# Kernel optimization log

Measured on AMD Instinct MI355X. Metric: run time of the kernel, lower is better.

The kernel has to match this reference:

```python
import jax, jax.numpy as jnp
import numpy as np

IN_DIM = 64
OUT_DIM = 128
GROUPS = 4
KS = 3
PAD = 1
SPLINE_ORDER = 3
GRID_SIZE = 5
GRID_K = GRID_SIZE + SPLINE_ORDER  # 8
GRID_LO, GRID_HI = -1.0, 1.0
_H = (GRID_HI - GRID_LO) / GRID_SIZE
GRID = jnp.linspace(GRID_LO - _H * SPLINE_ORDER, GRID_HI + _H * SPLINE_ORDER,
                    GRID_SIZE + 2 * SPLINE_ORDER + 1, dtype=jnp.float32)  # [14]
EPS = 1e-5


def _conv(x, w):
    # NCHW x OIHW -> NCHW, stride 1, dilation 1, padding PAD
    return jax.lax.conv_general_dilated(
        x, w, window_strides=(1, 1), padding=((PAD, PAD), (PAD, PAD)),
        dimension_numbers=('NCHW', 'OIHW', 'NCHW'))


def _bspline_bases(x):
    # Cox-de-Boor recursion; x: [B,C,H,W] -> [B, C*GRID_K, H, W]
    xu = x[..., None]  # [B,C,H,W,1]
    g = GRID
    bases = ((xu >= g[:-1]) & (xu < g[1:])).astype(x.dtype)  # [B,C,H,W,13]
    for k in range(1, SPLINE_ORDER + 1):
        left = g[:-(k + 1)]
        right = g[k:-1]
        delta = jnp.where(right == left, jnp.ones_like(right), right - left)
        bases = ((xu - left) / delta * bases[..., :-1]
                 + (g[k + 1:] - xu) / (g[k + 1:] - g[1:-k]) * bases[..., 1:])
    B, C, H, W, K = bases.shape  # K == GRID_K
    # moveaxis(-1, 2) then flatten(1, 2): channel-major, basis-minor ordering
    return jnp.moveaxis(bases, -1, 2).reshape(B, C * K, H, W)


def setup_inputs() -> dict:
    key = jax.random.key(0)
    k1, k2 = jax.random.split(key)
    x = jax.random.normal(k1, (8, IN_DIM, 64, 64), dtype=jnp.float32)
    # layer_weight: [out/g, (in/g)*(grid_k+1), ks, ks] = [32, 144, 3, 3]
    layer_weight = jax.random.normal(
        k2, (OUT_DIM // GROUPS, (IN_DIM // GROUPS) * (GRID_K + 1), KS, KS),
        dtype=jnp.float32) * 0.05
    prelu_w = jnp.full((GROUPS,), 0.25, dtype=jnp.float32)  # torch PReLU init
    return {"x": x, "layer_weight": layer_weight, "prelu_w": prelu_w}


def reference(x, layer_weight, prelu_w):
    cin_g = IN_DIM // GROUPS
    cout_g = OUT_DIM // GROUPS
    base_w = layer_weight[:, -cin_g:].reshape(cout_g, cin_g, KS, KS)
    spline_w = layer_weight[:, :-cin_g].reshape(cout_g, cin_g * GRID_K, KS, KS)
    outs = []
    for g in range(GROUPS):
        xg = x[:, g * cin_g:(g + 1) * cin_g]
        base_out = _conv(jax.nn.gelu(xg, approximate=False), base_w)
        spline_out = _conv(_bspline_bases(xg), spline_w)
        y = base_out + spline_out
        # InstanceNorm2d (affine=False): per-sample per-channel spatial norm
        mu = y.mean(axis=(2, 3), keepdims=True)
        var = y.var(axis=(2, 3), keepdims=True)
        y = (y - mu) / jnp.sqrt(var + EPS)
        # PReLU with scalar slope per group
        y = jnp.where(y >= 0, y, prelu_w[g] * y)
        outs.append(y)
    return jnp.concatenate(outs, axis=1)  # [B, OUT_DIM, H, W]
```

## Files before the change

kernel.cpp:

```cpp
#include <hip/hip_runtime.h>
#include <hip/hip_bf16.h>
#include <math.h>

typedef __attribute__((ext_vector_type(8))) short short8;
typedef __attribute__((ext_vector_type(4))) float f32x4;
typedef __attribute__((ext_vector_type(16))) float f32x16;
typedef unsigned int u32;
typedef unsigned long long u64;

__device__ __forceinline__ ushort f2bf(float f) {
    u32 u = __float_as_uint(f);
    return (ushort)((u + 0x7fffu + ((u >> 16) & 1u)) >> 16);
}

__global__ void wtrans(const float* __restrict__ lw, ushort* __restrict__ w2) {
    int t = blockIdx.x * 256 + threadIdx.x;
    if (t >= 5184) return;
    int l    = t & 63;
    int page = t >> 6;
    int ks  = page % 9;
    int tap = page / 9;
    int oc = l & 31;
    int kbase = ks * 16 + ((l >> 5) << 3);
    short8 v;
#pragma unroll
    for (int e = 0; e < 8; ++e) {
        int k = kbase + e;
        v[e] = (short)f2bf(lw[(oc * 144 + k) * 9 + tap]);
    }
    ((short8*)w2)[t] = v;
}

__global__ __launch_bounds__(256, 4) void kanconv(const float* __restrict__ x,
                                                  const ushort* __restrict__ w2,
                                                  ushort* __restrict__ yraw) {
    __shared__ __align__(16) ushort Fs[108 * 152];
    const int tid  = threadIdx.x;
    const int tile = blockIdx.x;
    const int b    = blockIdx.y;
    const int g    = blockIdx.z;
    const int h0 = (tile >> 2) * 4;
    const int w0 = (tile & 3) * 16;
    const float* xg = x + ((size_t)(b * 64 + g * 16)) * 4096;

    float xv[7];
    unsigned imgbits = 0;
#pragma unroll
    for (int it = 0; it < 7; ++it) {
        int e = it * 256 + tid;
        float v = 0.f;
        if (e < 1728) {
            int icg = e / 108;
            int p   = e - icg * 108;
            int py = p / 18, px = p - py * 18;
            int hy = h0 + py - 1, wx = w0 + px - 1;
            if (((unsigned)hy < 64u) && ((unsigned)wx < 64u)) {
                v = xg[icg * 4096 + hy * 64 + wx];
                imgbits |= (1u << it);
            }
        }
        xv[it] = v;
    }

#pragma unroll
    for (int it = 0; it < 7; ++it) {
        int e = it * 256 + tid;
        if (e < 1728) {
            int icg = e / 108;
            int p   = e - icg * 108;
            bool img = (imgbits >> it) & 1u;
            float v = xv[it];
            float tpos = (v + 2.2f) * 2.5f;
            float cf = floorf(tpos);
            int ci = (int)cf;
            float u = tpos - cf;
            float u2 = u * u, u3 = u2 * u, om = 1.f - u;
            const float s6 = 1.f / 6.f;
            float q0 = om * om * om * s6;
            float q1 = (4.f - 6.f * u2 + 3.f * u3) * s6;
            float q2 = (1.f + 3.f * u + 3.f * u2 - 3.f * u3) * s6;
            float q3 = u3 * s6;
            u64 Q =   (u64)f2bf(q0)
                    | ((u64)f2bf(q1) << 16)
                    | ((u64)f2bf(q2) << 32)
                    | ((u64)f2bf(q3) << 48);
            u64 lo = 0, hi = 0;
            if (img && ci >= 0 && ci <= 10) {
                int s = ci * 16 - 48;
                if (s < 0)        { lo = Q >> (-s); }
                else if (s < 64)  { lo = Q << s; hi = s ? (Q >> (64 - s)) : 0ull; }
                else              { hi = Q << (s - 64); }
            }
            union { u64 u64v[2]; short8 s8; } un;
            un.u64v[0] = lo; un.u64v[1] = hi;
            ushort* row = &Fs[p * 152];
            *(short8*)(row + icg * 8) = un.s8;
            float z  = v * 0.70710678118654752f;
            float az = fabsf(z);
            float tt = 1.f / fmaf(0.3275911f, az, 1.f);
            float poly = tt * fmaf(tt, fmaf(tt, fmaf(tt, fmaf(tt, 1.061405429f,
                          -1.453152027f), 1.421413741f), -0.284496736f),
                          0.254829592f);
            float er = 1.f - poly * __expf(-z * z);
            er = (z < 0.f) ? -er : er;
            float ge = 0.5f * v * (1.f + er);
            row[128 + icg] = f2bf(ge);
        }
    }
    __syncthreads();

    const int wv = tid >> 6;
    const int l  = tid & 63;
    const int la = l & 31, klo = l >> 5;
    const int p0row = la >> 4, p0col = la & 15;

    f32x16 accA, accB;
#pragma unroll
    for (int i = 0; i < 16; ++i) { accA[i] = 0.f; accB[i] = 0.f; }
    const short8* w8 = (const short8*)w2;

#pragma unroll
    for (int t2 = 0; t2 < 2; ++t2) {
        const int tap = wv * 2 + t2;
        const int kh = tap / 3, kw = tap - kh * 3;
        const ushort* fb0 = &Fs[((p0row + kh) * 18 + (p0col + kw)) * 152 + klo * 8];
        const ushort* fb1 = fb0 + 2 * 18 * 152;
        const short8* ap = w8 + tap * 576 + l;
#pragma unroll
        for (int ks = 0; ks < 9; ++ks) {
            short8 a   = ap[ks * 64];
            short8 bf0 = *(const short8*)(fb0 + ks * 16);
            short8 bf1 = *(const short8*)(fb1 + ks * 16);
            accA = __builtin_amdgcn_mfma_f32_32x32x16_bf16(a, bf0, accA, 0, 0, 0);
            accB = __builtin_amdgcn_mfma_f32_32x32x16_bf16(a, bf1, accB, 0, 0, 0);
        }
    }
    if (wv == 3) {
        const ushort* fb0 = &Fs[((p0row + 2) * 18 + (p0col + 2)) * 152 + klo * 8];
        const ushort* fb1 = fb0 + 2 * 18 * 152;
        const short8* ap = w8 + 8 * 576 + l;
#pragma unroll
        for (int ks = 0; ks < 9; ++ks) {
            short8 a   = ap[ks * 64];
            short8 bf0 = *(const short8*)(fb0 + ks * 16);
            short8 bf1 = *(const short8*)(fb1 + ks * 16);
            accA = __builtin_amdgcn_mfma_f32_32x32x16_bf16(a, bf0, accA, 0, 0, 0);
            accB = __builtin_amdgcn_mfma_f32_32x32x16_bf16(a, bf1, accB, 0, 0, 0);
        }
    }

    __syncthreads();
    float* comb = (float*)Fs;
    if (wv != 0) {
        float* cp = comb + ((wv - 1) * 64 + l) * 20;
        *(f32x4*)(cp + 0)  = f32x4{accA[0], accA[1], accA[2], accA[3]};
        *(f32x4*)(cp + 4)  = f32x4{accA[4], accA[5], accA[6], accA[7]};
        *(f32x4*)(cp + 8)  = f32x4{accA[8], accA[9], accA[10], accA[11]};
        *(f32x4*)(cp + 12) = f32x4{accA[12], accA[13], accA[14], accA[15]};
    }
    if (wv != 1) {
        int slot = (wv == 0) ? 3 : (2 + wv);
        float* cp = comb + (slot * 64 + l) * 20;
        *(f32x4*)(cp + 0)  = f32x4{accB[0], accB[1], accB[2], accB[3]};
        *(f32x4*)(cp + 4)  = f32x4{accB[4], accB[5], accB[6], accB[7]};
        *(f32x4*)(cp + 8)  = f32x4{accB[8], accB[9], accB[10], accB[11]};
        *(f32x4*)(cp + 12) = f32x4{accB[12], accB[13], accB[14], accB[15]};
    }
    __syncthreads();
    if (wv < 2) {
        f32x16 sum = (wv == 0) ? accA : accB;
        const int sbase = (wv == 0) ? 0 : 3;
#pragma unroll
        for (int s = 0; s < 3; ++s) {
            const float* cp = comb + ((sbase + s) * 64 + l) * 20;
            f32x4 c0 = *(const f32x4*)(cp + 0);
            f32x4 c1 = *(const f32x4*)(cp + 4);
            f32x4 c2 = *(const f32x4*)(cp + 8);
            f32x4 c3 = *(const f32x4*)(cp + 12);
#pragma unroll
            for (int r = 0; r < 4; ++r) {
                sum[r]      += c0[r];
                sum[r + 4]  += c1[r];
                sum[r + 8]  += c2[r];
                sum[r + 12] += c3[r];
            }
        }
        const int pix = wv * 32 + la;
        const int prow = pix >> 4, pcol = pix & 15;
        ushort* yb = yraw + (((size_t)b * 128 + g * 32) * 64 + h0 + prow) * 64
                          + w0 + pcol;
#pragma unroll
        for (int r = 0; r < 16; ++r) {
            int oc = (r & 3) + 8 * (r >> 2) + 4 * klo;
            yb[(size_t)oc * 4096] = f2bf(sum[r]);
        }
    }
}

__global__ __launch_bounds__(256) void instnorm(const ushort* __restrict__ yraw,
                                                float* __restrict__ y,
                                                const float* __restrict__ prelu) {
    const int blk = blockIdx.x;
    const int tid = threadIdx.x;
    const short8* rp = (const short8*)(yraw + (size_t)blk * 4096);
    short8 a = rp[tid * 2], c = rp[tid * 2 + 1];
    float v[16];
#pragma unroll
    for (int j = 0; j < 8; ++j) {
        v[j]     = __uint_as_float(((u32)(ushort)a[j]) << 16);
        v[8 + j] = __uint_as_float(((u32)(ushort)c[j]) << 16);
    }
    float s = 0.f, s2 = 0.f;
#pragma unroll
    for (int j = 0; j < 16; ++j) { s += v[j]; s2 += v[j] * v[j]; }
#pragma unroll
    for (int off = 32; off > 0; off >>= 1) {
        s  += __shfl_down(s, off);
        s2 += __shfl_down(s2, off);
    }
    __shared__ float red[8];
    int wave = tid >> 6;
    if ((tid & 63) == 0) { red[wave] = s; red[4 + wave] = s2; }
    __syncthreads();
    float S  = red[0] + red[1] + red[2] + red[3];
    float S2 = red[4] + red[5] + red[6] + red[7];
    float mean = S * (1.0f / 4096.0f);
    float var  = S2 * (1.0f / 4096.0f) - mean * mean;
    float rstd = rsqrtf(var + 1e-5f);
    float slope = prelu[(blk >> 5) & 3];
    float4* op = (float4*)(y + (size_t)blk * 4096) + tid * 4;
#pragma unroll
    for (int k = 0; k < 4; ++k) {
        float4 o;
        float t;
        t = (v[k * 4 + 0] - mean) * rstd; o.x = t >= 0.f ? t : slope * t;
        t = (v[k * 4 + 1] - mean) * rstd; o.y = t >= 0.f ? t : slope * t;
        t = (v[k * 4 + 2] - mean) * rstd; o.z = t >= 0.f ? t : slope * t;
        t = (v[k * 4 + 3] - mean) * rstd; o.w = t >= 0.f ? t : slope * t;
        op[k] = o;
    }
}

extern "C" void kernel_launch(void* const* d_in, const int* in_sizes, int n_in,
                              void* d_out, int out_size, void* d_ws, size_t ws_size,
                              hipStream_t stream) {
    const float* x     = (const float*)d_in[0];
    const float* lw    = (const float*)d_in[1];
    const float* prelu = (const float*)d_in[2];
    float*  out  = (float*)d_out;
    ushort* w2   = (ushort*)d_ws;
    ushort* yraw = (ushort*)((char*)d_ws + 92160);

    wtrans<<<21, 256, 0, stream>>>(lw, w2);
    dim3 grid(64, 8, 4);
    kanconv<<<grid, 256, 0, stream>>>(x, w2, yraw);
    instnorm<<<1024, 256, 0, stream>>>(yraw, out, prelu);
}
```

Before: 40.70 us.

## Split input channels across blocks and sum bf16 partials in instnorm

```diff
diff --git a/kernel.cpp b/kernel.cpp
--- a/kernel.cpp
+++ b/kernel.cpp
@@ -12,44 +12,53 @@
     u32 u = __float_as_uint(f);
     return (ushort)((u + 0x7fffu + ((u >> 16) & 1u)) >> 16);
 }
+__device__ __forceinline__ float bf2f(ushort h) {
+    return __uint_as_float(((u32)h) << 16);
+}
 
 __global__ void wtrans(const float* __restrict__ lw, ushort* __restrict__ w2) {
     int t = blockIdx.x * 256 + threadIdx.x;
-    if (t >= 5184) return;
+    if (t >= 5760) return;
     int l    = t & 63;
     int page = t >> 6;
-    int ks  = page % 9;
-    int tap = page / 9;
+    int ks  = page % 5;
+    int tap = (page / 5) % 9;
+    int kk  = page / 45;
     int oc = l & 31;
     int kbase = ks * 16 + ((l >> 5) << 3);
     short8 v;
 #pragma unroll
     for (int e = 0; e < 8; ++e) {
         int k = kbase + e;
-        v[e] = (short)f2bf(lw[(oc * 144 + k) * 9 + tap]);
+        float val = 0.f;
+        if (k < 64)       val = lw[(oc * 144 + kk * 64 + k) * 9 + tap];
+        else if (k < 72)  val = lw[(oc * 144 + 128 + kk * 8 + (k - 64)) * 9 + tap];
+        v[e] = (short)f2bf(val);
     }
     ((short8*)w2)[t] = v;
 }
 
-__global__ __launch_bounds__(256, 4) void kanconv(const float* __restrict__ x,
+__global__ __launch_bounds__(128, 4) void kanconv(const float* __restrict__ x,
                                                   const ushort* __restrict__ w2,
                                                   ushort* __restrict__ yraw) {
-    __shared__ __align__(16) ushort Fs[108 * 152];
+    __shared__ __align__(16) ushort Fs[108 * 88];
     const int tid  = threadIdx.x;
     const int tile = blockIdx.x;
     const int b    = blockIdx.y;
-    const int g    = blockIdx.z;
+    const int gz   = blockIdx.z;
+    const int g    = gz & 3;
+    const int kk   = gz >> 2;
     const int h0 = (tile >> 2) * 4;
     const int w0 = (tile & 3) * 16;
-    const float* xg = x + ((size_t)(b * 64 + g * 16)) * 4096;
+    const float* xg = x + ((size_t)(b * 64 + g * 16 + kk * 8)) * 4096;
 
     float xv[7];
     unsigned imgbits = 0;
 #pragma unroll
     for (int it = 0; it < 7; ++it) {
-        int e = it * 256 + tid;
+        int e = it * 128 + tid;
         float v = 0.f;
-        if (e < 1728) {
+        if (e < 864) {
             int icg = e / 108;
             int p   = e - icg * 108;
             int py = p / 18, px = p - py * 18;
@@ -64,8 +73,8 @@
 
 #pragma unroll
     for (int it = 0; it < 7; ++it) {
-        int e = it * 256 + tid;
-        if (e < 1728) {
+        int e = it * 128 + tid;
+        if (e < 864) {
             int icg = e / 108;
             int p   = e - icg * 108;
             bool img = (imgbits >> it) & 1u;
@@ -93,7 +102,7 @@
             }
             union { u64 u64v[2]; short8 s8; } un;
             un.u64v[0] = lo; un.u64v[1] = hi;
-            ushort* row = &Fs[p * 152];
+            ushort* row = &Fs[p * 88];
             *(short8*)(row + icg * 8) = un.s8;
             float z  = v * 0.70710678118654752f;
             float az = fabsf(z);
@@ -104,96 +113,45 @@
             float er = 1.f - poly * __expf(-z * z);
             er = (z < 0.f) ? -er : er;
             float ge = 0.5f * v * (1.f + er);
-            row[128 + icg] = f2bf(ge);
+            row[64 + icg] = f2bf(ge);
         }
+    }
+    {
+        short8 z8 = {0, 0, 0, 0, 0, 0, 0, 0};
+        if (tid < 108) *(short8*)&Fs[tid * 88 + 72] = z8;
     }
     __syncthreads();
 
     const int wv = tid >> 6;
     const int l  = tid & 63;
     const int la = l & 31, klo = l >> 5;
-    const int p0row = la >> 4, p0col = la & 15;
-
-    f32x16 accA, accB;
-#pragma unroll
-    for (int i = 0; i < 16; ++i) { accA[i] = 0.f; accB[i] = 0.f; }
-    const short8* w8 = (const short8*)w2;
-
-#pragma unroll
-    for (int t2 = 0; t2 < 2; ++t2) {
-        const int tap = wv * 2 + t2;
+    const int pix = wv * 32 + la;
+    const int prow = pix >> 4, pcol = pix & 15;
+
+    f32x16 acc;
+#pragma unroll
+    for (int i = 0; i < 16; ++i) acc[i] = 0.f;
+    const short8* w8 = (const short8*)w2 + kk * 45 * 64;
+
+#pragma unroll
+    for (int tap = 0; tap < 9; ++tap) {
         const int kh = tap / 3, kw = tap - kh * 3;
-        const ushort* fb0 = &Fs[((p0row + kh) * 18 + (p0col + kw)) * 152 + klo * 8];
-        const ushort* fb1 = fb0 + 2 * 18 * 152;
-        const short8* ap = w8 + tap * 576 + l;
-#pragma unroll
-        for (int ks = 0; ks < 9; ++ks) {
-            short8 a   = ap[ks * 64];
-            short8 bf0 = *(const short8*)(fb0 + ks * 16);
-            short8 bf1 = *(const short8*)(fb1 + ks * 16);
-            accA = __builtin_amdgcn_mfma_f32_32x32x16_bf16(a, bf0, accA, 0, 0, 0);
-            accB = __builtin_amdgcn_mfma_f32_32x32x16_bf16(a, bf1, accB, 0, 0, 0);
+        const ushort* fb = &Fs[((prow + kh) * 18 + (pcol + kw)) * 88 + klo * 8];
+        const short8* ap = w8 + tap * 5 * 64 + l;
+#pragma unroll
+        for (int ks = 0; ks < 5; ++ks) {
+            short8 a  = ap[ks * 64];
+            short8 bf = *(const short8*)(fb + ks * 16);
+            acc = __builtin_amdgcn_mfma_f32_32x32x16_bf16(a, bf, acc, 0, 0, 0);
         }
     }
-    if (wv == 3) {
-        const ushort* fb0 = &Fs[((p0row + 2) * 18 + (p0col + 2)) * 152 + klo * 8];
-        const ushort* fb1 = fb0 + 2 * 18 * 152;
-        const short8* ap = w8 + 8 * 576 + l;
-#pragma unroll
-        for (int ks = 0; ks < 9; ++ks) {
-            short8 a   = ap[ks * 64];
-            short8 bf0 = *(const short8*)(fb0 + ks * 16);
-            short8 bf1 = *(const short8*)(fb1 + ks * 16);
-            accA = __builtin_amdgcn_mfma_f32_32x32x16_bf16(a, bf0, accA, 0, 0, 0);
-            accB = __builtin_amdgcn_mfma_f32_32x32x16_bf16(a, bf1, accB, 0, 0, 0);
-        }
-    }
-
-    __syncthreads();
-    float* comb = (float*)Fs;
-    if (wv != 0) {
-        float* cp = comb + ((wv - 1) * 64 + l) * 20;
-        *(f32x4*)(cp + 0)  = f32x4{accA[0], accA[1], accA[2], accA[3]};
-        *(f32x4*)(cp + 4)  = f32x4{accA[4], accA[5], accA[6], accA[7]};
-        *(f32x4*)(cp + 8)  = f32x4{accA[8], accA[9], accA[10], accA[11]};
-        *(f32x4*)(cp + 12) = f32x4{accA[12], accA[13], accA[14], accA[15]};
-    }
-    if (wv != 1) {
-        int slot = (wv == 0) ? 3 : (2 + wv);
-        float* cp = comb + (slot * 64 + l) * 20;
-        *(f32x4*)(cp + 0)  = f32x4{accB[0], accB[1], accB[2], accB[3]};
-        *(f32x4*)(cp + 4)  = f32x4{accB[4], accB[5], accB[6], accB[7]};
-        *(f32x4*)(cp + 8)  = f32x4{accB[8], accB[9], accB[10], accB[11]};
-        *(f32x4*)(cp + 12) = f32x4{accB[12], accB[13], accB[14], accB[15]};
-    }
-    __syncthreads();
-    if (wv < 2) {
-        f32x16 sum = (wv == 0) ? accA : accB;
-        const int sbase = (wv == 0) ? 0 : 3;
-#pragma unroll
-        for (int s = 0; s < 3; ++s) {
-            const float* cp = comb + ((sbase + s) * 64 + l) * 20;
-            f32x4 c0 = *(const f32x4*)(cp + 0);
-            f32x4 c1 = *(const f32x4*)(cp + 4);
-            f32x4 c2 = *(const f32x4*)(cp + 8);
-            f32x4 c3 = *(const f32x4*)(cp + 12);
-#pragma unroll
-            for (int r = 0; r < 4; ++r) {
-                sum[r]      += c0[r];
-                sum[r + 4]  += c1[r];
-                sum[r + 8]  += c2[r];
-                sum[r + 12] += c3[r];
-            }
-        }
-        const int pix = wv * 32 + la;
-        const int prow = pix >> 4, pcol = pix & 15;
-        ushort* yb = yraw + (((size_t)b * 128 + g * 32) * 64 + h0 + prow) * 64
-                          + w0 + pcol;
-#pragma unroll
-        for (int r = 0; r < 16; ++r) {
-            int oc = (r & 3) + 8 * (r >> 2) + 4 * klo;
-            yb[(size_t)oc * 4096] = f2bf(sum[r]);
-        }
+
+    ushort* yb = yraw + (size_t)kk * 4194304
+               + (((size_t)b * 128 + g * 32) * 64 + h0 + prow) * 64 + w0 + pcol;
+#pragma unroll
+    for (int r = 0; r < 16; ++r) {
+        int oc = (r & 3) + 8 * (r >> 2) + 4 * klo;
+        yb[(size_t)oc * 4096] = f2bf(acc[r]);
     }
 }
 
@@ -202,13 +160,15 @@
                                                 const float* __restrict__ prelu) {
     const int blk = blockIdx.x;
     const int tid = threadIdx.x;
-    const short8* rp = (const short8*)(yraw + (size_t)blk * 4096);
-    short8 a = rp[tid * 2], c = rp[tid * 2 + 1];
+    const short8* rp0 = (const short8*)(yraw + (size_t)blk * 4096);
+    const short8* rp1 = (const short8*)(yraw + 4194304 + (size_t)blk * 4096);
+    short8 a0 = rp0[tid * 2], a1 = rp0[tid * 2 + 1];
+    short8 c0 = rp1[tid * 2], c1 = rp1[tid * 2 + 1];
     float v[16];
 #pragma unroll
     for (int j = 0; j < 8; ++j) {
-        v[j]     = __uint_as_float(((u32)(ushort)a[j]) << 16);
-        v[8 + j] = __uint_as_float(((u32)(ushort)c[j]) << 16);
+        v[j]     = bf2f((ushort)a0[j]) + bf2f((ushort)c0[j]);
+        v[8 + j] = bf2f((ushort)a1[j]) + bf2f((ushort)c1[j]);
     }
     float s = 0.f, s2 = 0.f;
 #pragma unroll
@@ -251,8 +211,8 @@
     ushort* w2   = (ushort*)d_ws;
     ushort* yraw = (ushort*)((char*)d_ws + 92160);
 
-    wtrans<<<21, 256, 0, stream>>>(lw, w2);
-    dim3 grid(64, 8, 4);
-    kanconv<<<grid, 256, 0, stream>>>(x, w2, yraw);
+    wtrans<<<23, 256, 0, stream>>>(lw, w2);
+    dim3 grid(64, 8, 8);
+    kanconv<<<grid, 128, 0, stream>>>(x, w2, yraw);
     instnorm<<<1024, 256, 0, stream>>>(yraw, out, prelu);
 }
```

Result: slower. 43.53 us (+7.0%).

## Overlap second-half feature staging with MFMA on first-half channels

Applied to the files above, without the earlier changes.

```diff
diff --git a/kernel.cpp b/kernel.cpp
--- a/kernel.cpp
+++ b/kernel.cpp
@@ -11,6 +11,14 @@
 __device__ __forceinline__ ushort f2bf(float f) {
     u32 u = __float_as_uint(f);
     return (ushort)((u + 0x7fffu + ((u >> 16) & 1u)) >> 16);
+}
+__device__ __forceinline__ float bf2f(ushort h) {
+    return __uint_as_float(((u32)h) << 16);
+}
+__device__ __forceinline__ u32 cvtpk_bf16(float a, float b) {
+    u32 r;
+    asm("v_cvt_pk_bf16_f32 %0, %1, %2" : "=v"(r) : "v"(a), "v"(b));
+    return r;
 }
 
 __global__ void wtrans(const float* __restrict__ lw, ushort* __restrict__ w2) {
@@ -34,7 +42,7 @@
 __global__ __launch_bounds__(256, 4) void kanconv(const float* __restrict__ x,
                                                   const ushort* __restrict__ w2,
                                                   ushort* __restrict__ yraw) {
-    __shared__ __align__(16) ushort Fs[108 * 152];
+    __shared__ __align__(16) ushort Fs[109 * 152];
     const int tid  = threadIdx.x;
     const int tile = blockIdx.x;
     const int b    = blockIdx.y;
@@ -43,111 +51,119 @@
     const int w0 = (tile & 3) * 16;
     const float* xg = x + ((size_t)(b * 64 + g * 16)) * 4096;
 
-    float xv[7];
+    float xv1[4], xv2[4];
     unsigned imgbits = 0;
 #pragma unroll
-    for (int it = 0; it < 7; ++it) {
+    for (int it = 0; it < 4; ++it) {
         int e = it * 256 + tid;
-        float v = 0.f;
-        if (e < 1728) {
-            int icg = e / 108;
-            int p   = e - icg * 108;
-            int py = p / 18, px = p - py * 18;
-            int hy = h0 + py - 1, wx = w0 + px - 1;
-            if (((unsigned)hy < 64u) && ((unsigned)wx < 64u)) {
-                v = xg[icg * 4096 + hy * 64 + wx];
-                imgbits |= (1u << it);
-            }
-        }
-        xv[it] = v;
-    }
-
-#pragma unroll
-    for (int it = 0; it < 7; ++it) {
-        int e = it * 256 + tid;
-        if (e < 1728) {
-            int icg = e / 108;
-            int p   = e - icg * 108;
-            bool img = (imgbits >> it) & 1u;
-            float v = xv[it];
-            float tpos = (v + 2.2f) * 2.5f;
-            float cf = floorf(tpos);
-            int ci = (int)cf;
-            float u = tpos - cf;
-            float u2 = u * u, u3 = u2 * u, om = 1.f - u;
-            const float s6 = 1.f / 6.f;
-            float q0 = om * om * om * s6;
-            float q1 = (4.f - 6.f * u2 + 3.f * u3) * s6;
-            float q2 = (1.f + 3.f * u + 3.f * u2 - 3.f * u3) * s6;
-            float q3 = u3 * s6;
-            u64 Q =   (u64)f2bf(q0)
-                    | ((u64)f2bf(q1) << 16)
-                    | ((u64)f2bf(q2) << 32)
-                    | ((u64)f2bf(q3) << 48);
-            u64 lo = 0, hi = 0;
-            if (img && ci >= 0 && ci <= 10) {
-                int s = ci * 16 - 48;
-                if (s < 0)        { lo = Q >> (-s); }
-                else if (s < 64)  { lo = Q << s; hi = s ? (Q >> (64 - s)) : 0ull; }
-                else              { hi = Q << (s - 64); }
-            }
-            union { u64 u64v[2]; short8 s8; } un;
-            un.u64v[0] = lo; un.u64v[1] = hi;
-            ushort* row = &Fs[p * 152];
-            *(short8*)(row + icg * 8) = un.s8;
-            float z  = v * 0.70710678118654752f;
-            float az = fabsf(z);
-            float tt = 1.f / fmaf(0.3275911f, az, 1.f);
-            float poly = tt * fmaf(tt, fmaf(tt, fmaf(tt, fmaf(tt, 1.061405429f,
-                          -1.453152027f), 1.421413741f), -0.284496736f),
-                          0.254829592f);
-            float er = 1.f - poly * __expf(-z * z);
-            er = (z < 0.f) ? -er : er;
-            float ge = 0.5f * v * (1.f + er);
-            row[128 + icg] = f2bf(ge);
-        }
-    }
+        int icg = e / 108;
+        int p   = e - icg * 108;
+        int py = p / 18, px = p - py * 18;
+        int hy = h0 + py - 1, wx = w0 + px - 1;
+        bool valid = (e < 864) && ((unsigned)hy < 64u) && ((unsigned)wx < 64u);
+        int off = valid ? (icg * 4096 + hy * 64 + wx) : 0;
+        float a = xg[off];
+        float c = xg[off + 8 * 4096];
+        if (!valid) { a = 0.f; c = 0.f; } else { imgbits |= (1u << it); }
+        xv1[it] = a;
+        xv2[it] = c;
+    }
+
+#define STAGE(V, IMGF, ROWP, SLOT)                                            \
+    do {                                                                      \
+        float v_ = (V);                                                       \
+        float tpos_ = (v_ + 2.2f) * 2.5f;                                     \
+        float cf_ = floorf(tpos_);                                            \
+        int ci_ = (int)cf_;                                                   \
+        float u_ = tpos_ - cf_;                                               \
+        float u2_ = u_ * u_, u3_ = u2_ * u_, om_ = 1.f - u_;                  \
+        float q0_ = om_ * om_ * om_ * (1.f / 6.f);                            \
+        float q1_ = (4.f - 6.f * u2_ + 3.f * u3_) * (1.f / 6.f);              \
+        float q2_ = (1.f + 3.f * u_ + 3.f * u2_ - 3.f * u3_) * (1.f / 6.f);   \
+        float q3_ = u3_ * (1.f / 6.f);                                        \
+        u64 Q_ = (u64)cvtpk_bf16(q0_, q1_)                                    \
+               | ((u64)cvtpk_bf16(q2_, q3_) << 32);                           \
+        u64 lo_ = 0, hi_ = 0;                                                 \
+        if ((IMGF) && ci_ >= 0 && ci_ <= 10) {                                \
+            int s_ = ci_ * 16 - 48;                                           \
+            if (s_ < 0)       { lo_ = Q_ >> (-s_); }                          \
+            else if (s_ < 64) { lo_ = Q_ << s_;                               \
+                                hi_ = s_ ? (Q_ >> (64 - s_)) : 0ull; }        \
+            else              { hi_ = Q_ << (s_ - 64); }                      \
+        }                                                                     \
+        union { u64 q[2]; short8 s8; } un_;                                   \
+        un_.q[0] = lo_; un_.q[1] = hi_;                                       \
+        ushort* row_ = &Fs[(ROWP) * 152];                                     \
+        *(short8*)(row_ + (SLOT) * 8) = un_.s8;                               \
+        float x3_ = v_ * v_ * v_;                                             \
+        float t2_ = fmaf(0.0713548163f, x3_, 1.5957691216f * v_);             \
+        float e2_ = __expf(t2_);                                              \
+        float th_ = 1.f - 2.f / (e2_ + 1.f);                                  \
+        float ge_ = 0.5f * v_ * (1.f + th_);                                  \
+        row_[128 + (SLOT)] = f2bf(ge_);                                       \
+    } while (0)
+
+#define STAGE_IT(IT, XV, SB)                                                  \
+    do {                                                                      \
+        int e_ = (IT) * 256 + tid;                                            \
+        int icg_ = e_ / 108;                                                  \
+        int p_ = e_ - icg_ * 108;                                             \
+        int rowp_ = (e_ < 864) ? p_ : 108;         \
+        bool im_ = (imgbits >> (IT)) & 1u;                                    \
+        STAGE((XV)[IT], im_, rowp_, icg_ + (SB));                             \
+    } while (0)
+
+    STAGE_IT(0, xv1, 0);
+    STAGE_IT(1, xv1, 0);
+    STAGE_IT(2, xv1, 0);
+    STAGE_IT(3, xv1, 0);
     __syncthreads();
 
     const int wv = tid >> 6;
     const int l  = tid & 63;
     const int la = l & 31, klo = l >> 5;
     const int p0row = la >> 4, p0col = la & 15;
+    const short8* w8 = (const short8*)w2;
 
     f32x16 accA, accB;
 #pragma unroll
     for (int i = 0; i < 16; ++i) { accA[i] = 0.f; accB[i] = 0.f; }
-    const short8* w8 = (const short8*)w2;
-
-#pragma unroll
-    for (int t2 = 0; t2 < 2; ++t2) {
-        const int tap = wv * 2 + t2;
-        const int kh = tap / 3, kw = tap - kh * 3;
-        const ushort* fb0 = &Fs[((p0row + kh) * 18 + (p0col + kw)) * 152 + klo * 8];
-        const ushort* fb1 = fb0 + 2 * 18 * 152;
-        const short8* ap = w8 + tap * 576 + l;
-#pragma unroll
-        for (int ks = 0; ks < 9; ++ks) {
-            short8 a   = ap[ks * 64];
-            short8 bf0 = *(const short8*)(fb0 + ks * 16);
-            short8 bf1 = *(const short8*)(fb1 + ks * 16);
-            accA = __builtin_amdgcn_mfma_f32_32x32x16_bf16(a, bf0, accA, 0, 0, 0);
-            accB = __builtin_amdgcn_mfma_f32_32x32x16_bf16(a, bf1, accB, 0, 0, 0);
-        }
-    }
-    if (wv == 3) {
-        const ushort* fb0 = &Fs[((p0row + 2) * 18 + (p0col + 2)) * 152 + klo * 8];
-        const ushort* fb1 = fb0 + 2 * 18 * 152;
-        const short8* ap = w8 + 8 * 576 + l;
-#pragma unroll
-        for (int ks = 0; ks < 9; ++ks) {
-            short8 a   = ap[ks * 64];
-            short8 bf0 = *(const short8*)(fb0 + ks * 16);
-            short8 bf1 = *(const short8*)(fb1 + ks * 16);
-            accA = __builtin_amdgcn_mfma_f32_32x32x16_bf16(a, bf0, accA, 0, 0, 0);
-            accB = __builtin_amdgcn_mfma_f32_32x32x16_bf16(a, bf1, accB, 0, 0, 0);
-        }
-    }
+
+#define TAPKS(TAP, K0, K1)                                                     \
+    do {                                                                       \
+        const int kh_ = (TAP) / 3, kw_ = (TAP) - kh_ * 3;                      \
+        const ushort* fb0_ =                                                   \
+            &Fs[((p0row + kh_) * 18 + (p0col + kw_)) * 152 + klo * 8];         \
+        const ushort* fb1_ = fb0_ + 2 * 18 * 152;                              \
+        const short8* ap_ = w8 + (TAP) * 576 + l;                              \
+        _Pragma("unroll")                                                      \
+        for (int ks_ = (K0); ks_ < (K1); ++ks_) {                              \
+            short8 a_  = ap_[ks_ * 64];                                        \
+            short8 b0_ = *(const short8*)(fb0_ + ks_ * 16);                    \
+            short8 b1_ = *(const short8*)(fb1_ + ks_ * 16);                    \
+            accA = __builtin_amdgcn_mfma_f32_32x32x16_bf16(a_, b0_, accA, 0, 0, 0); \
+            accB = __builtin_amdgcn_mfma_f32_32x32x16_bf16(a_, b1_, accB, 0, 0, 0); \
+        }                                                                      \
+    } while (0)
+
+    const int t0 = wv * 2, t1 = wv * 2 + 1;
+
+    STAGE_IT(0, xv2, 8);
+    STAGE_IT(1, xv2, 8);
+    TAPKS(t0, 0, 2);
+    STAGE_IT(2, xv2, 8);
+    TAPKS(t0, 2, 4);
+    STAGE_IT(3, xv2, 8);
+    TAPKS(t1, 0, 4);
+    if (wv == 3) TAPKS(8, 0, 4);
+    __syncthreads();
+
+    TAPKS(t0, 4, 9);
+    TAPKS(t1, 4, 9);
+    if (wv == 3) TAPKS(8, 4, 9);
+#undef TAPKS
+#undef STAGE_IT
+#undef STAGE
 
     __syncthreads();
     float* comb = (float*)Fs;
@@ -207,8 +223,8 @@
     float v[16];
 #pragma unroll
     for (int j = 0; j < 8; ++j) {
-        v[j]     = __uint_as_float(((u32)(ushort)a[j]) << 16);
-        v[8 + j] = __uint_as_float(((u32)(ushort)c[j]) << 16);
+        v[j]     = bf2f((ushort)a[j]);
+        v[8 + j] = bf2f((ushort)c[j]);
     }
     float s = 0.f, s2 = 0.f;
 #pragma unroll
```

Measured after the change: 39.87 us. 1.02x faster.
